# Performance work log

Measured on AMD Instinct MI355X. Metric: run time of the kernel, lower is better.

Reference implementation:

```python
import jax, jax.numpy as jnp
import numpy as np


@jax.custom_vjp
def binarize(w):
    # BNN-style sign binarization: forward sign(w), backward straight-through (identity)
    return jnp.sign(w)


def _binarize_fwd(w):
    return jnp.sign(w), None


def _binarize_bwd(_, g):
    return (g,)


binarize.defvjp(_binarize_fwd, _binarize_bwd)


def setup_inputs() -> dict:
    key = jax.random.key(0)
    kx, kw = jax.random.split(key)
    N, IN, OUT = 4096, 4096, 4096
    x = jax.random.normal(kx, (N, IN), dtype=jnp.float32)
    # xavier_normal init: std = sqrt(2 / (fan_in + fan_out))
    std = (2.0 / (IN + OUT)) ** 0.5
    W = jax.random.normal(kw, (OUT, IN), dtype=jnp.float32) * std
    b = jnp.zeros((OUT,), dtype=jnp.float32)
    return {"x": x, "W": W, "b": b}


def reference(x, W, b):
    wb = binarize(W)                      # [OUT, IN] in {-1, 0, +1}
    return x @ wb.T + b                   # [N, OUT]
```

## Files before the change

### kernel.cpp

```cpp
#include <hip/hip_runtime.h>
#include <hip/hip_bf16.h>
#include <stdint.h>

typedef __attribute__((ext_vector_type(8))) short short8;
typedef __attribute__((ext_vector_type(8))) unsigned short ushort8;
typedef __attribute__((ext_vector_type(4))) float f32x4;


__device__ inline unsigned short f2bf_rne(float f) {
    union { float f; unsigned int u; } v; v.f = f;
    unsigned int u = v.u;
    unsigned int r = u + 0x7FFFu + ((u >> 16) & 1u);
    return (unsigned short)(r >> 16);
}

__global__ __launch_bounds__(256) void cvt_x_kernel(const float* __restrict__ in,
                                                    unsigned short* __restrict__ out,
                                                    int n8) {
    int i = blockIdx.x * blockDim.x + threadIdx.x;
    if (i >= n8) return;
    const float4* p = reinterpret_cast<const float4*>(in) + (size_t)i * 2;
    float4 a = p[0];
    float4 b = p[1];
    ushort8 o;
    o[0] = f2bf_rne(a.x); o[1] = f2bf_rne(a.y); o[2] = f2bf_rne(a.z); o[3] = f2bf_rne(a.w);
    o[4] = f2bf_rne(b.x); o[5] = f2bf_rne(b.y); o[6] = f2bf_rne(b.z); o[7] = f2bf_rne(b.w);
    *reinterpret_cast<ushort8*>(out + (size_t)i * 8) = o;
}

__device__ inline unsigned short signbf(float f) {
    return (f > 0.0f) ? (unsigned short)0x3F80u
         : (f < 0.0f) ? (unsigned short)0xBF80u
                      : (unsigned short)0u;
}

__global__ __launch_bounds__(256) void cvt_w_kernel(const float* __restrict__ in,
                                                    unsigned short* __restrict__ out,
                                                    int n8) {
    int i = blockIdx.x * blockDim.x + threadIdx.x;
    if (i >= n8) return;
    const float4* p = reinterpret_cast<const float4*>(in) + (size_t)i * 2;
    float4 a = p[0];
    float4 b = p[1];
    ushort8 o;
    o[0] = signbf(a.x); o[1] = signbf(a.y); o[2] = signbf(a.z); o[3] = signbf(a.w);
    o[4] = signbf(b.x); o[5] = signbf(b.y); o[6] = signbf(b.z); o[7] = signbf(b.w);
    *reinterpret_cast<ushort8*>(out + (size_t)i * 8) = o;
}


#define BM 128
#define BN 128
#define BK 32

__device__ inline void gload_lds16(const void* g, void* l) {
    __builtin_amdgcn_global_load_lds(
        (const __attribute__((address_space(1))) unsigned int*)g,
        (__attribute__((address_space(3))) unsigned int*)l,
        16, 0, 0);
}

__global__ __launch_bounds__(256) void gemm_bt_bias(
    const unsigned short* __restrict__ A,
    const unsigned short* __restrict__ B,
    const float* __restrict__ bias,
    float* __restrict__ C,
    int M, int N, int K)
{
    __shared__ unsigned short sA[BM * BK];
    __shared__ unsigned short sB[BN * BK];

    const int tid  = threadIdx.x;
    const int wid  = tid >> 6;
    const int lane = tid & 63;
    const int brow = blockIdx.y * BM;
    const int bcol = blockIdx.x * BN;
    const int wr = wid >> 1;
    const int wc = wid & 1;

    const int st_r  = (lane >> 2);
    const int st_c  = (lane & 3) * 8;

    f32x4 acc[4][4];
#pragma unroll
    for (int m = 0; m < 4; ++m)
#pragma unroll
        for (int n = 0; n < 4; ++n)
            acc[m][n] = (f32x4){0.f, 0.f, 0.f, 0.f};

    for (int k0 = 0; k0 < K; k0 += BK) {
        __syncthreads();
#pragma unroll
        for (int j = 0; j < 2; ++j) {
            const int c = wid * 2 + j;
            const int r = c * 16 + st_r;
            const unsigned short* ga = A + (size_t)(brow + r) * K + k0 + st_c;
            gload_lds16(ga, sA + c * 512);
            const unsigned short* gb = B + (size_t)(bcol + r) * K + k0 + st_c;
            gload_lds16(gb, sB + c * 512);
        }
        __syncthreads();

        short8 af[4], bf[4];
        const int kc = (lane >> 4) * 8;
#pragma unroll
        for (int m = 0; m < 4; ++m) {
            const int row = wr * 64 + m * 16 + (lane & 15);
            af[m] = *reinterpret_cast<const short8*>(&sA[row * BK + kc]);
        }
#pragma unroll
        for (int n = 0; n < 4; ++n) {
            const int row = wc * 64 + n * 16 + (lane & 15);
            bf[n] = *reinterpret_cast<const short8*>(&sB[row * BK + kc]);
        }
#pragma unroll
        for (int m = 0; m < 4; ++m)
#pragma unroll
            for (int n = 0; n < 4; ++n)
                acc[m][n] = __builtin_amdgcn_mfma_f32_16x16x32_bf16(
                    af[m], bf[n], acc[m][n], 0, 0, 0);
    }

#pragma unroll
    for (int n = 0; n < 4; ++n) {
        const int col = bcol + wc * 64 + n * 16 + (lane & 15);
        const float bv = bias[col];
#pragma unroll
        for (int m = 0; m < 4; ++m) {
            const int row0 = brow + wr * 64 + m * 16 + (lane >> 4) * 4;
#pragma unroll
            for (int j = 0; j < 4; ++j) {
                C[(size_t)(row0 + j) * N + col] = acc[m][n][j] + bv;
            }
        }
    }
}


extern "C" void kernel_launch(void* const* d_in, const int* in_sizes, int n_in,
                              void* d_out, int out_size, void* d_ws, size_t ws_size,
                              hipStream_t stream) {
    const float* x  = (const float*)d_in[0];
    const float* W  = (const float*)d_in[1];
    const float* bv = (const float*)d_in[2];
    float* out = (float*)d_out;

    const int OUT = in_sizes[2];
    const int IN  = in_sizes[1] / OUT;
    const int M   = in_sizes[0] / IN;

    unsigned short* xb = (unsigned short*)d_ws;
    unsigned short* wb = xb + (size_t)M * IN;

    {
        const int n8 = (M * IN) / 8;
        cvt_x_kernel<<<(n8 + 255) / 256, 256, 0, stream>>>(x, xb, n8);
    }
    {
        const int n8 = (OUT * IN) / 8;
        cvt_w_kernel<<<(n8 + 255) / 256, 256, 0, stream>>>(W, wb, n8);
    }
    gemm_bt_bias<<<dim3(OUT / BN, M / BM), 256, 0, stream>>>(
        xb, wb, bv, out, M, OUT, IN);
}
```

Baseline: 360.7 us.

## Rewrite GEMM as 256x256 double-buffered tile with swizzled LDS and XCD remap

Replaces the 128x128x32 single-buffered GEMM with a 256x256x64 tile kernel of 512 threads that double-buffers LDS, issuing global-to-LDS loads for the next K tile while MFMAs run on the current one. LDS rows are XOR-swizzled to avoid bank conflicts. Work is split into phases separated by barriers with raised wave priority around MFMA bursts, and block IDs are remapped across the 8 XCDs for cache locality. This targets load latency, sync stalls and low arithmetic intensity, at the cost of 128KB of dynamic LDS (which limits occupancy) and heavier register use.

```diff
diff --git a/kernel.cpp b/kernel.cpp
--- a/kernel.cpp
+++ b/kernel.cpp
@@ -5,6 +5,7 @@
 typedef __attribute__((ext_vector_type(8))) short short8;
 typedef __attribute__((ext_vector_type(8))) unsigned short ushort8;
 typedef __attribute__((ext_vector_type(4))) float f32x4;
+typedef unsigned short ushort_t;
 
 
 __device__ inline unsigned short f2bf_rne(float f) {
@@ -49,85 +50,185 @@
 }
 
 
-#define BM 128
-#define BN 128
-#define BK 32
-
-__device__ inline void gload_lds16(const void* g, void* l) {
+#define BM 256
+#define BN 256
+#define BK 64
+
+__device__ __forceinline__ void gload_lds16(const void* g, void* l) {
     __builtin_amdgcn_global_load_lds(
         (const __attribute__((address_space(1))) unsigned int*)g,
         (__attribute__((address_space(3))) unsigned int*)l,
         16, 0, 0);
 }
 
-__global__ __launch_bounds__(256) void gemm_bt_bias(
-    const unsigned short* __restrict__ A,
-    const unsigned short* __restrict__ B,
+__device__ __forceinline__ void phase_barrier() {
+    __builtin_amdgcn_sched_barrier(0);
+    __builtin_amdgcn_s_barrier();
+    __builtin_amdgcn_sched_barrier(0);
+}
+
+__device__ __forceinline__ void stage_tile(
+    const ushort_t* __restrict__ A, const ushort_t* __restrict__ B,
+    ushort_t* ldsA, ushort_t* ldsB,
+    int brow, int bcol, int kbase, int K,
+    int wid, int srow, int scol)
+{
+#pragma unroll
+    for (int h = 0; h < 2; ++h)
+#pragma unroll
+        for (int r = 0; r < 2; ++r) {
+            const int rowoff = h * 128 + r * 64 + wid * 8;
+            const ushort_t* ga = A + (size_t)(brow + rowoff + srow) * K + kbase + scol;
+            gload_lds16(ga, ldsA + rowoff * 64);
+            const ushort_t* gb = B + (size_t)(bcol + rowoff + srow) * K + kbase + scol;
+            gload_lds16(gb, ldsB + rowoff * 64);
+        }
+}
+
+__global__ __launch_bounds__(512, 2) void gemm8_bt_bias(
+    const ushort_t* __restrict__ A,
+    const ushort_t* __restrict__ B,
     const float* __restrict__ bias,
     float* __restrict__ C,
-    int M, int N, int K)
+    int M, int N, int K, int tn_n)
 {
-    __shared__ unsigned short sA[BM * BK];
-    __shared__ unsigned short sB[BN * BK];
+    extern __shared__ ushort_t lds[];
 
     const int tid  = threadIdx.x;
     const int wid  = tid >> 6;
     const int lane = tid & 63;
-    const int brow = blockIdx.y * BM;
-    const int bcol = blockIdx.x * BN;
-    const int wr = wid >> 1;
-    const int wc = wid & 1;
-
-    const int st_r  = (lane >> 2);
-    const int st_c  = (lane & 3) * 8;
-
-    f32x4 acc[4][4];
-#pragma unroll
-    for (int m = 0; m < 4; ++m)
+    const int wr = wid >> 2;
+    const int wc = wid & 3;
+
+    unsigned nwg = gridDim.x, orig = blockIdx.x;
+    unsigned qd = nwg >> 3, rm = nwg & 7u;
+    unsigned xcd = orig & 7u, sub = orig >> 3;
+    unsigned id = (xcd < rm ? xcd * (qd + 1) : rm * (qd + 1) + (xcd - rm) * qd) + sub;
+    const int tm = (int)(id / (unsigned)tn_n);
+    const int tn = (int)(id % (unsigned)tn_n);
+    const int brow = tm * BM;
+    const int bcol = tn * BN;
+
+    const int nt = K / BK;
+
+    const int srow = lane >> 3;
+    const int scol = ((lane & 7) ^ srow) << 3;
+
+    const int r15 = lane & 15;
+    const int hi2 = lane >> 4;
+    const int l7  = lane & 7;
+    const int sK0 = ((hi2) ^ l7) * 8;
+    const int sK1 = ((4 + hi2) ^ l7) * 8;
+    const int bRow = (wc & 1) * 64;
+
+    f32x4 acc[8][4];
+#pragma unroll
+    for (int m = 0; m < 8; ++m)
 #pragma unroll
         for (int n = 0; n < 4; ++n)
             acc[m][n] = (f32x4){0.f, 0.f, 0.f, 0.f};
 
-    for (int k0 = 0; k0 < K; k0 += BK) {
+    stage_tile(A, B, lds, lds + 32768, brow, bcol, 0, K, wid, srow, scol);
+    __syncthreads();
+
+    short8 aF[2][4], bF[2][4];
+
+#pragma unroll 2
+    for (int t = 0; t < nt; ++t) {
+        const int cur = t & 1;
+        const ushort_t* aC = lds + cur * 16384 + wr * 8192;
+        const ushort_t* bC = lds + 32768 + cur * 16384 + (wc >> 1) * 8192;
+
+        if (t + 1 < nt) {
+            const int nxt = cur ^ 1;
+            stage_tile(A, B, lds + nxt * 16384, lds + 32768 + nxt * 16384,
+                       brow, bcol, (t + 1) * BK, K, wid, srow, scol);
+        }
+
+#pragma unroll
+        for (int i = 0; i < 4; ++i) {
+            aF[0][i] = *reinterpret_cast<const short8*>(aC + (i * 16 + r15) * 64 + sK0);
+            aF[1][i] = *reinterpret_cast<const short8*>(aC + (i * 16 + r15) * 64 + sK1);
+        }
+#pragma unroll
+        for (int n = 0; n < 2; ++n) {
+            bF[0][n] = *reinterpret_cast<const short8*>(bC + (bRow + n * 16 + r15) * 64 + sK0);
+            bF[1][n] = *reinterpret_cast<const short8*>(bC + (bRow + n * 16 + r15) * 64 + sK1);
+        }
+        phase_barrier();
+        __builtin_amdgcn_s_setprio(1);
+#pragma unroll
+        for (int i = 0; i < 4; ++i)
+#pragma unroll
+            for (int j = 0; j < 2; ++j) {
+                f32x4 c = acc[i][j];
+                c = __builtin_amdgcn_mfma_f32_16x16x32_bf16(aF[0][i], bF[0][j], c, 0, 0, 0);
+                c = __builtin_amdgcn_mfma_f32_16x16x32_bf16(aF[1][i], bF[1][j], c, 0, 0, 0);
+                acc[i][j] = c;
+            }
+        __builtin_amdgcn_s_setprio(0);
+        phase_barrier();
+
+#pragma unroll
+        for (int n = 2; n < 4; ++n) {
+            bF[0][n] = *reinterpret_cast<const short8*>(bC + (bRow + n * 16 + r15) * 64 + sK0);
+            bF[1][n] = *reinterpret_cast<const short8*>(bC + (bRow + n * 16 + r15) * 64 + sK1);
+        }
+        phase_barrier();
+        __builtin_amdgcn_s_setprio(1);
+#pragma unroll
+        for (int i = 0; i < 4; ++i)
+#pragma unroll
+            for (int j = 2; j < 4; ++j) {
+                f32x4 c = acc[i][j];
+                c = __builtin_amdgcn_mfma_f32_16x16x32_bf16(aF[0][i], bF[0][j], c, 0, 0, 0);
+                c = __builtin_amdgcn_mfma_f32_16x16x32_bf16(aF[1][i], bF[1][j], c, 0, 0, 0);
+                acc[i][j] = c;
+            }
+        __builtin_amdgcn_s_setprio(0);
+        phase_barrier();
+
+#pragma unroll
+        for (int i = 0; i < 4; ++i) {
+            aF[0][i] = *reinterpret_cast<const short8*>(aC + ((4 + i) * 16 + r15) * 64 + sK0);
+            aF[1][i] = *reinterpret_cast<const short8*>(aC + ((4 + i) * 16 + r15) * 64 + sK1);
+        }
+        phase_barrier();
+        __builtin_amdgcn_s_setprio(1);
+#pragma unroll
+        for (int i = 0; i < 4; ++i)
+#pragma unroll
+            for (int j = 0; j < 2; ++j) {
+                f32x4 c = acc[4 + i][j];
+                c = __builtin_amdgcn_mfma_f32_16x16x32_bf16(aF[0][i], bF[0][j], c, 0, 0, 0);
+                c = __builtin_amdgcn_mfma_f32_16x16x32_bf16(aF[1][i], bF[1][j], c, 0, 0, 0);
+                acc[4 + i][j] = c;
+            }
+        __builtin_amdgcn_s_setprio(0);
+        phase_barrier();
+
+        __builtin_amdgcn_s_setprio(1);
+#pragma unroll
+        for (int i = 0; i < 4; ++i)
+#pragma unroll
+            for (int j = 2; j < 4; ++j) {
+                f32x4 c = acc[4 + i][j];
+                c = __builtin_amdgcn_mfma_f32_16x16x32_bf16(aF[0][i], bF[0][j], c, 0, 0, 0);
+                c = __builtin_amdgcn_mfma_f32_16x16x32_bf16(aF[1][i], bF[1][j], c, 0, 0, 0);
+                acc[4 + i][j] = c;
+            }
+        __builtin_amdgcn_s_setprio(0);
+
         __syncthreads();
-#pragma unroll
-        for (int j = 0; j < 2; ++j) {
-            const int c = wid * 2 + j;
-            const int r = c * 16 + st_r;
-            const unsigned short* ga = A + (size_t)(brow + r) * K + k0 + st_c;
-            gload_lds16(ga, sA + c * 512);
-            const unsigned short* gb = B + (size_t)(bcol + r) * K + k0 + st_c;
-            gload_lds16(gb, sB + c * 512);
-        }
-        __syncthreads();
-
-        short8 af[4], bf[4];
-        const int kc = (lane >> 4) * 8;
-#pragma unroll
-        for (int m = 0; m < 4; ++m) {
-            const int row = wr * 64 + m * 16 + (lane & 15);
-            af[m] = *reinterpret_cast<const short8*>(&sA[row * BK + kc]);
-        }
-#pragma unroll
-        for (int n = 0; n < 4; ++n) {
-            const int row = wc * 64 + n * 16 + (lane & 15);
-            bf[n] = *reinterpret_cast<const short8*>(&sB[row * BK + kc]);
-        }
-#pragma unroll
-        for (int m = 0; m < 4; ++m)
-#pragma unroll
-            for (int n = 0; n < 4; ++n)
-                acc[m][n] = __builtin_amdgcn_mfma_f32_16x16x32_bf16(
-                    af[m], bf[n], acc[m][n], 0, 0, 0);
     }
 
 #pragma unroll
     for (int n = 0; n < 4; ++n) {
-        const int col = bcol + wc * 64 + n * 16 + (lane & 15);
+        const int col = bcol + wc * 64 + n * 16 + r15;
         const float bv = bias[col];
 #pragma unroll
-        for (int m = 0; m < 4; ++m) {
-            const int row0 = brow + wr * 64 + m * 16 + (lane >> 4) * 4;
+        for (int m = 0; m < 8; ++m) {
+            const int row0 = brow + wr * 128 + m * 16 + hi2 * 4;
 #pragma unroll
             for (int j = 0; j < 4; ++j) {
                 C[(size_t)(row0 + j) * N + col] = acc[m][n][j] + bv;
@@ -160,6 +261,11 @@
         const int n8 = (OUT * IN) / 8;
         cvt_w_kernel<<<(n8 + 255) / 256, 256, 0, stream>>>(W, wb, n8);
     }
-    gemm_bt_bias<<<dim3(OUT / BN, M / BM), 256, 0, stream>>>(
-        xb, wb, bv, out, M, OUT, IN);
-}
+
+    const int tn_n = OUT / BN;
+    const int tm_n = M / BM;
+    const int nblk = tn_n * tm_n;
+    (void)hipFuncSetAttribute((const void*)gemm8_bt_bias,
+                              hipFuncAttributeMaxDynamicSharedMemorySize, 131072);
+    gemm8_bt_bias<<<nblk, 512, 131072, stream>>>(xb, wb, bv, out, M, OUT, IN, tn_n);
+}
```

New measurement: 290.4 us. 1.24x faster.
